# Kernel optimization log

Hardware: AMD Instinct MI355X
Metric: run time of the kernel (lower is better)

## Reference

```python
import jax, jax.numpy as jnp
import numpy as np

B, W, KD, NC, D, NN, NH, AD, HOPS = 512, 4, 64, 32, 256, 16, 8, 32, 4
DH = D // NH
DFF = 4 * D
P = B * W + B
ROLE_WRITER, ROLE_QUERY = 0, 1


def setup_inputs() -> dict:
    key = jax.random.key(0)
    ks = iter(jax.random.split(key, 40))
    f = lambda shape, s=0.02: jax.random.normal(next(ks), shape, dtype=jnp.float32) * s
    inp = {
        'query_keys': jax.random.normal(next(ks), (B, KD), dtype=jnp.float32),
        'writer_keys': jax.random.normal(next(ks), (B, W, KD), dtype=jnp.float32),
        'key_proj_w': f((KD, D)), 'key_proj_b': jnp.zeros((D,), jnp.float32),
        'class_embed': f((NC, D)), 'role_embed': f((3, D)), 'start_node_embed': f((NN, D)),
        'input_ln_g': jnp.ones((D,), jnp.float32), 'input_ln_b': jnp.zeros((D,), jnp.float32),
        'ln1_g': jnp.ones((NN, D), jnp.float32), 'ln1_b': jnp.zeros((NN, D), jnp.float32),
        'wqkv': f((NN, D, 3 * D)), 'bqkv': jnp.zeros((NN, 3 * D), jnp.float32),
        'wo': f((NN, D, D)), 'bo': jnp.zeros((NN, D), jnp.float32),
        'ln2_g': jnp.ones((NN, D), jnp.float32), 'ln2_b': jnp.zeros((NN, D), jnp.float32),
        'w_fc1': f((NN, D, DFF)), 'b_fc1': jnp.zeros((NN, DFF), jnp.float32),
        'w_fc2': f((NN, DFF, D)), 'b_fc2': jnp.zeros((NN, D), jnp.float32),
        'delta_w': jnp.zeros((D, D), jnp.float32), 'delta_b': jnp.zeros((D,), jnp.float32),
        'dir_w': f((D, D)), 'dir_b': jnp.zeros((D,), jnp.float32),
        'mag_w': f((D, 1)), 'mag_b': jnp.full((1,), 2.5, jnp.float32),
        'out_w': f((D, NC)), 'out_b': jnp.zeros((NC,), jnp.float32),
        'address_table': jax.random.normal(next(ks), (NN, AD), dtype=jnp.float32),
        'query_start_nodes': jax.random.randint(next(ks), (B,), 0, NN),
        'writer_labels': jax.random.randint(next(ks), (B, W), 0, NC),
        'writer_start_nodes': jax.random.randint(next(ks), (B, W), 0, NN),
    }
    return inp


def _ln(x):
    m = jnp.mean(x, -1, keepdims=True)
    v = jnp.var(x, -1, keepdims=True)
    return (x - m) * jax.lax.rsqrt(v + 1e-5)


def _forward(query_keys, writer_keys, key_proj_w, key_proj_b, class_embed, role_embed,
             start_node_embed, input_ln_g, input_ln_b, ln1_g, ln1_b, wqkv, bqkv, wo, bo,
             ln2_g, ln2_b, w_fc1, b_fc1, w_fc2, b_fc2, delta_w, delta_b, dir_w, dir_b,
             mag_w, mag_b, out_w, out_b, address_table,
             query_start_nodes, writer_labels, writer_start_nodes):
    # ---- encode writers (encode_writers) ----
    fk = writer_keys.reshape(-1, KD)          # [B*W, KD]
    fl = writer_labels.reshape(-1)            # [B*W]
    fs = writer_start_nodes.reshape(-1)       # [B*W]
    learned_w = fk @ key_proj_w + key_proj_b + class_embed[fl] + start_node_embed[fs] + role_embed[ROLE_WRITER]
    sw = jnp.zeros_like(learned_w).at[:, :KD].set(fk)
    sw = sw.at[:, KD:KD + NC].set(jax.nn.one_hot(fl, NC, dtype=learned_w.dtype))
    enc_w = _ln(learned_w) * input_ln_g + input_ln_b + sw
    # ---- encode queries (encode_queries) ----
    learned_q = query_keys @ key_proj_w + key_proj_b + start_node_embed[query_start_nodes] + role_embed[ROLE_QUERY]
    sq = jnp.zeros_like(learned_q).at[:, :KD].set(query_keys)
    enc_q = _ln(learned_q) * input_ln_g + input_ln_b + sq

    h = jnp.concatenate([enc_w, enc_q], axis=0)          # [P, D]
    node = jnp.concatenate([fs, query_start_nodes], 0)   # [P] current compute node per packet

    inv_sqrt_dh = 1.0 / np.sqrt(DH).astype(np.float32)
    for _ in range(HOPS):
        oh = jax.nn.one_hot(node, NN, dtype=h.dtype)      # [P, NN] dispatch weights

        def pnl(x, Wn, bn):
            # per-node linear: gather-compute-scatter via MoE-style dense dispatch
            xe = jnp.einsum('pn,pd->npd', oh, x)          # [NN, P, din]
            ye = jnp.einsum('npd,ndf->npf', xe, Wn)       # [NN, P, dout]
            return jnp.einsum('npf,pn->pf', ye, oh) + oh @ bn

        # ComputeNodeCell: pre-LN attention among packets at the same node
        x = _ln(h) * (oh @ ln1_g) + oh @ ln1_b
        qkv = pnl(x, wqkv, bqkv)                          # [P, 3D]
        q, k, v = jnp.split(qkv, 3, axis=-1)
        q = q.reshape(P, NH, DH); k = k.reshape(P, NH, DH); v = v.reshape(P, NH, DH)
        scores = jnp.einsum('phd,qhd->hpq', q, k) * inv_sqrt_dh   # [NH, P, P]
        same = node[:, None] == node[None, :]
        scores = jnp.where(same[None], scores, -1e9)
        attn = jax.nn.softmax(scores, axis=-1)
        ao = jnp.einsum('hpq,qhd->phd', attn, v).reshape(P, D)
        h = h + pnl(ao, wo, bo)
        # MLP block
        x2 = _ln(h) * (oh @ ln2_g) + oh @ ln2_b
        h = h + pnl(jax.nn.gelu(pnl(x2, w_fc1, b_fc1)), w_fc2, b_fc2)
        # routing heads: pick next node from address table, apply gated delta
        direction = h @ dir_w + dir_b
        node = jnp.argmax(direction[:, :AD] @ address_table.T, axis=-1)
        h = h + (h @ delta_w + delta_b) * jax.nn.sigmoid(h @ mag_w + mag_b)

    return h @ out_w + out_b                              # [P, NC] per-packet logits


def reference(query_keys, writer_keys, key_proj_w, key_proj_b, class_embed, role_embed,
              start_node_embed, input_ln_g, input_ln_b, ln1_g, ln1_b, wqkv, bqkv, wo, bo,
              ln2_g, ln2_b, w_fc1, b_fc1, w_fc2, b_fc2, delta_w, delta_b, dir_w, dir_b,
              mag_w, mag_b, out_w, out_b, address_table,
              query_start_nodes, writer_labels, writer_start_nodes):
    return _forward(query_keys, writer_keys, key_proj_w, key_proj_b, class_embed, role_embed,
                    start_node_embed, input_ln_g, input_ln_b, ln1_g, ln1_b, wqkv, bqkv, wo, bo,
                    ln2_g, ln2_b, w_fc1, b_fc1, w_fc2, b_fc2, delta_w, delta_b, dir_w, dir_b,
                    mag_w, mag_b, out_w, out_b, address_table,
                    query_start_nodes, writer_labels, writer_start_nodes)
```

## Files before the change

### kernel.cpp

```cpp
#include <hip/hip_runtime.h>
#include <math.h>

#define B_    512
#define W_    4
#define KD_   64
#define NC_   32
#define D_    256
#define NN_   16
#define NH_   8
#define AD_   32
#define HOPS_ 4
#define DH_   32
#define DFF_  1024
#define P_    2560
#define BW_   2048
#define MAXT2_ 176
#define PS_   (P_ + 16)

#define INV_SQRT_DH 0.17677669529663687f

typedef __attribute__((ext_vector_type(8))) short short8v;
typedef __attribute__((ext_vector_type(4))) float f32x4;

__device__ __forceinline__ unsigned short bf16_rne(float f) {
  unsigned u = __float_as_uint(f);
  unsigned r = (u + 0x7fffu + ((u >> 16) & 1u)) >> 16;
  return (unsigned short)r;
}
__device__ __forceinline__ void split2(float v, unsigned short& h, unsigned short& l) {
  unsigned short hb = bf16_rne(v);
  float hf = __uint_as_float(((unsigned)hb) << 16);
  h = hb;
  l = bf16_rne(v - hf);
}

__device__ __forceinline__ float block_sum256(float v, float* red) {
#pragma unroll
  for (int off = 32; off > 0; off >>= 1) v += __shfl_xor(v, off, 64);
  int wid = threadIdx.x >> 6;
  if ((threadIdx.x & 63) == 0) red[wid] = v;
  __syncthreads();
  float s = red[0] + red[1] + red[2] + red[3];
  __syncthreads();
  return s;
}

__device__ __forceinline__ float gelu_tanh(float v) {
  float u = 0.7978845608028654f * (v + 0.044715f * v * v * v);
  return 0.5f * v * (1.0f + tanhf(u));
}

__global__ __launch_bounds__(256) void padzero_kernel(unsigned short* __restrict__ xh,
                                                      unsigned short* __restrict__ xl,
                                                      unsigned short* __restrict__ ffh,
                                                      unsigned short* __restrict__ ffl) {
  int t = threadIdx.x;
  for (int i = t; i < 16 * D_; i += 256) {
    xh[(size_t)P_ * D_ + i] = 0;
    xl[(size_t)P_ * D_ + i] = 0;
  }
  for (int i = t; i < 16 * DFF_; i += 256) {
    ffh[(size_t)P_ * DFF_ + i] = 0;
    ffl[(size_t)P_ * DFF_ + i] = 0;
  }
}

__global__ __launch_bounds__(256) void encode_kernel(
    const float* __restrict__ query_keys, const float* __restrict__ writer_keys,
    const float* __restrict__ kpw, const float* __restrict__ kpb,
    const float* __restrict__ ce, const float* __restrict__ re,
    const float* __restrict__ sne, const float* __restrict__ ilg,
    const float* __restrict__ ilb, const int* __restrict__ qsn,
    const int* __restrict__ wl, const int* __restrict__ wsn,
    float* __restrict__ h, int* __restrict__ node) {
  int p = blockIdx.x, t = threadIdx.x;
  __shared__ float fk[KD_];
  __shared__ float red[4];
  const float* key;
  int lab = -1, sn, role;
  if (p < BW_) { key = writer_keys + (size_t)p * KD_; lab = wl[p]; sn = wsn[p]; role = 0; }
  else { int b = p - BW_; key = query_keys + (size_t)b * KD_; sn = qsn[b]; role = 1; }
  if (t < KD_) fk[t] = key[t];
  __syncthreads();

  float acc = kpb[t] + sne[sn * D_ + t] + re[role * D_ + t];
  if (lab >= 0) acc += ce[lab * D_ + t];
#pragma unroll 8
  for (int i = 0; i < KD_; i++) acc += fk[i] * kpw[i * D_ + t];

  float mean = block_sum256(acc, red) * (1.0f / D_);
  float d = acc - mean;
  float var = block_sum256(d * d, red) * (1.0f / D_);
  float xn = d * (1.0f / sqrtf(var + 1e-5f));

  float sw = 0.0f;
  if (t < KD_) sw = fk[t];
  else if (lab >= 0 && t < KD_ + NC_) sw = (t - KD_ == lab) ? 1.0f : 0.0f;

  h[(size_t)p * D_ + t] = xn * ilg[t] + ilb[t] + sw;
  if (t == 0) node[p] = sn;
}

__global__ __launch_bounds__(256) void sort_kernel(const int* __restrict__ node,
                                                   int* __restrict__ order,
                                                   int* __restrict__ offs,
                                                   int* __restrict__ cnts,
                                                   int* __restrict__ tnode16,
                                                   int* __restrict__ tstart16,
                                                   int* __restrict__ tend16,
                                                   int* __restrict__ ntiles16) {
  __shared__ int c[NN_], o[NN_], cur[NN_];
  int t = threadIdx.x;
  if (t < NN_) c[t] = 0;
  __syncthreads();
  for (int p = t; p < P_; p += 256) atomicAdd(&c[node[p]], 1);
  __syncthreads();
  if (t == 0) {
    int s = 0;
    for (int n = 0; n < NN_; n++) { o[n] = s; cur[n] = s; s += c[n]; }
    int i16 = 0;
    for (int n = 0; n < NN_; n++) {
      int e = o[n] + c[n];
      for (int m0 = o[n]; m0 < e; m0 += 16) {
        tnode16[i16] = n; tstart16[i16] = m0; tend16[i16] = e; i16++;
      }
    }
    ntiles16[0] = i16;
  }
  __syncthreads();
  if (t < NN_) { cnts[t] = c[t]; offs[t] = o[t]; }
  for (int p = t; p < P_; p += 256) {
    int r = atomicAdd(&cur[node[p]], 1);
    order[r] = p;
  }
}

__global__ __launch_bounds__(256) void ln_affine(const float* __restrict__ h,
                                                 const float* __restrict__ g,
                                                 const float* __restrict__ b,
                                                 const int* __restrict__ node,
                                                 const int* __restrict__ order,
                                                 unsigned short* __restrict__ xh,
                                                 unsigned short* __restrict__ xl) {
  int sp = blockIdx.x * 4 + (threadIdx.x >> 6);
  int lane = threadIdx.x & 63;
  int p = order[sp];
  int n = node[p];
  float4 v = *(const float4*)&h[(size_t)p * D_ + lane * 4];
  float s = v.x + v.y + v.z + v.w;
#pragma unroll
  for (int off = 32; off > 0; off >>= 1) s += __shfl_xor(s, off, 64);
  float mean = s * (1.0f / D_);
  float4 d = make_float4(v.x - mean, v.y - mean, v.z - mean, v.w - mean);
  float vr = d.x * d.x + d.y * d.y + d.z * d.z + d.w * d.w;
#pragma unroll
  for (int off = 32; off > 0; off >>= 1) vr += __shfl_xor(vr, off, 64);
  float inv = 1.0f / sqrtf(vr * (1.0f / D_) + 1e-5f);
  float4 gg = *(const float4*)&g[n * D_ + lane * 4];
  float4 bb = *(const float4*)&b[n * D_ + lane * 4];
  float o[4];
  o[0] = d.x * inv * gg.x + bb.x;
  o[1] = d.y * inv * gg.y + bb.y;
  o[2] = d.z * inv * gg.z + bb.z;
  o[3] = d.w * inv * gg.w + bb.w;
  ushort4 oh, ol;
  split2(o[0], oh.x, ol.x);
  split2(o[1], oh.y, ol.y);
  split2(o[2], oh.z, ol.z);
  split2(o[3], oh.w, ol.w);
  *(ushort4*)&xh[(size_t)sp * D_ + lane * 4] = oh;
  *(ushort4*)&xl[(size_t)sp * D_ + lane * 4] = ol;
}

template <int K, int C>
__global__ __launch_bounds__(256) void wprep(const float* __restrict__ W,
                                             unsigned short* __restrict__ th,
                                             unsigned short* __restrict__ tl) {
  __shared__ float ld[32][33];
  int n = blockIdx.z;
  int k0 = blockIdx.x * 32, c0 = blockIdx.y * 32;
  int tx = threadIdx.x & 31, ty = threadIdx.x >> 5;
  const float* Wn = W + (size_t)n * K * C;
#pragma unroll
  for (int i = 0; i < 32; i += 8)
    ld[i + ty][tx] = Wn[(size_t)(k0 + i + ty) * C + c0 + tx];
  __syncthreads();
#pragma unroll
  for (int i = 0; i < 32; i += 8) {
    float v = ld[tx][i + ty];
    unsigned short hh, ll;
    split2(v, hh, ll);
    size_t off = ((size_t)n * C + c0 + i + ty) * K + k0 + tx;
    th[off] = hh;
    tl[off] = ll;
  }
}

template <int DIN, int DOUT, int ACT, int RESID, int SPLITOUT, int DENSE, int HSPLIT>
__global__ __launch_bounds__(256) void gmfma(
    const unsigned short* __restrict__ xh, const unsigned short* __restrict__ xl,
    const unsigned short* __restrict__ wth, const unsigned short* __restrict__ wtl,
    const float* __restrict__ bias, float* __restrict__ outf,
    unsigned short* __restrict__ outh, unsigned short* __restrict__ outl,
    unsigned short* __restrict__ houth, unsigned short* __restrict__ houtl,
    const int* __restrict__ order, const int* __restrict__ tnode,
    const int* __restrict__ tstart, const int* __restrict__ tend,
    const int* __restrict__ ntiles) {
  constexpr int NCH = DIN / 64;
  __shared__ unsigned short ws[2][2][64][64];

  int gx = gridDim.x;
  int bid = blockIdx.x;
  int ti = (bid & 7) * (gx >> 3) + (bid >> 3);
  int n, s0, rows;
  if (DENSE) {
    n = 0;
    s0 = ti * 16;
    rows = 16;
  } else {
    if (ti >= ntiles[0]) return;
    n = tnode[ti];
    s0 = tstart[ti];
    rows = tend[ti] - s0;
    if (rows <= 0) return;
    if (rows > 16) rows = 16;
  }

  int tid = threadIdx.x;
  int wv = tid >> 6;
  int lane = tid & 63;
  int r16 = lane & 15;
  int kg = lane >> 4;
  int jb = blockIdx.y * 64;

  const unsigned short* wsrc[4];
  int sj[4], c0j[4];
#pragma unroll
  for (int jj = 0; jj < 4; jj++) {
    int j = wv * 4 + jj;
    int s = j >> 3;
    int c0 = (j & 7) * 8;
    int c = c0 + (lane >> 3);
    int e = (lane & 7) ^ (c & 7);
    wsrc[jj] = ((e & 4) ? wtl : wth) +
               ((size_t)(n * DOUT + jb + c)) * DIN + s * 32 + (e & 3) * 8;
    sj[jj] = s;
    c0j[jj] = c0;
  }
  auto stage = [&](int buf, int kbase) {
#pragma unroll
    for (int jj = 0; jj < 4; jj++) {
      __builtin_amdgcn_global_load_lds(
          (const __attribute__((address_space(1))) unsigned int*)(wsrc[jj] + kbase),
          (__attribute__((address_space(3))) unsigned int*)&ws[buf][sj[jj]][c0j[jj]][0],
          16, 0, 0);
    }
  };

  const unsigned short* pah = xh + (size_t)(s0 + r16) * DIN + kg * 8;
  const unsigned short* pal = xl + (size_t)(s0 + r16) * DIN + kg * 8;

  short8v ah[2], al[2], nh[2], nl[2];
  auto afetch = [&](int kbase, short8v (&h_)[2], short8v (&l_)[2]) {
#pragma unroll
    for (int s = 0; s < 2; s++) {
      h_[s] = *(const short8v*)(pah + kbase + s * 32);
      l_[s] = *(const short8v*)(pal + kbase + s * 32);
    }
  };

  f32x4 acc0 = {0.f, 0.f, 0.f, 0.f};
  f32x4 acc1 = acc0, acc2 = acc0;
  int lcol = wv * 16 + r16;
  int ghi_ = (kg ^ (r16 & 7)) * 8;
  int glo_ = ((4 + kg) ^ (r16 & 7)) * 8;

  stage(0, 0);
  afetch(0, ah, al);
  __syncthreads();

  for (int ch = 0; ch < NCH; ch++) {
    int cur = ch & 1;
    if (ch + 1 < NCH) {
      stage(cur ^ 1, (ch + 1) * 64);
      afetch((ch + 1) * 64, nh, nl);
    }
#pragma unroll
    for (int s = 0; s < 2; s++) {
      short8v bh = *(const short8v*)&ws[cur][s][lcol][ghi_];
      short8v bl = *(const short8v*)&ws[cur][s][lcol][glo_];
      acc0 = __builtin_amdgcn_mfma_f32_16x16x32_bf16(ah[s], bh, acc0, 0, 0, 0);
      acc1 = __builtin_amdgcn_mfma_f32_16x16x32_bf16(ah[s], bl, acc1, 0, 0, 0);
      acc2 = __builtin_amdgcn_mfma_f32_16x16x32_bf16(al[s], bh, acc2, 0, 0, 0);
    }
    __syncthreads();
    if (ch + 1 < NCH) {
#pragma unroll
      for (int s = 0; s < 2; s++) { ah[s] = nh[s]; al[s] = nl[s]; }
    }
  }

  int jcol = jb + wv * 16;
  float bv = bias[(size_t)n * DOUT + jcol + r16];
#pragma unroll
  for (int rg = 0; rg < 4; rg++) {
    int r = kg * 4 + rg;
    if (r >= rows) continue;
    float v = acc0[rg] + acc1[rg] + acc2[rg] + bv;
    if (ACT) v = gelu_tanh(v);
    if (SPLITOUT) {
      size_t off = (size_t)(s0 + r) * DOUT + jcol + r16;
      unsigned short hh, ll;
      split2(v, hh, ll);
      outh[off] = hh;
      outl[off] = ll;
    } else if (RESID) {
      int pp = DENSE ? (s0 + r) : order[s0 + r];
      size_t oidx = (size_t)pp * DOUT + jcol + r16;
      float nv = outf[oidx] + v;
      outf[oidx] = nv;
      if (HSPLIT) {
        unsigned short hh, ll;
        split2(nv, hh, ll);
        houth[oidx] = hh;
        houtl[oidx] = ll;
      }
    } else {
      outf[(size_t)(s0 + r) * DOUT + jcol + r16] = v;
    }
  }
}

#define ATS 36
__global__ __launch_bounds__(256) void attn_kernel(const float* __restrict__ qkv,
                                                   const int* __restrict__ node,
                                                   const int* __restrict__ order,
                                                   const int* __restrict__ offs,
                                                   const int* __restrict__ cnts,
                                                   unsigned short* __restrict__ aoh,
                                                   unsigned short* __restrict__ aol) {
  __shared__ float qs[32 * ATS];
  __shared__ float kts[2][32 * ATS];
  __shared__ float vs[2][32 * ATS];
  __shared__ float ps[32 * ATS];
  __shared__ int glo[32], ghi[32];

  int t = threadIdx.x;
  int r = t >> 3;
  int j4 = (t & 7) * 4;
  int r0 = blockIdx.x * 32;
  int hd = blockIdx.y;

  if (t < 32) {
    int n = node[order[r0 + t]];
    glo[t] = offs[n];
    ghi[t] = offs[n] + cnts[n];
  }
  __syncthreads();

  {
    const float* qp = &qkv[(size_t)(r0 + r) * 768 + hd * 32 + j4];
    float4 q4 = *(const float4*)qp;
    q4.x *= INV_SQRT_DH; q4.y *= INV_SQRT_DH; q4.z *= INV_SQRT_DH; q4.w *= INV_SQRT_DH;
    *(float4*)&qs[r * ATS + j4] = q4;
  }

  int lo = glo[0];
  int hi = ghi[31];
  int myglo = glo[r], myghi = ghi[r];
  int nt = (hi - lo + 31) >> 5;

  {
    int sj = lo + r;
    float4 k4 = {0.f, 0.f, 0.f, 0.f}, v4 = {0.f, 0.f, 0.f, 0.f};
    if (sj < hi) {
      const float* kp = &qkv[(size_t)sj * 768 + 256 + hd * 32 + j4];
      k4 = *(const float4*)kp;
      v4 = *(const float4*)(kp + 256);
    }
    kts[0][(j4 + 0) * ATS + r] = k4.x;
    kts[0][(j4 + 1) * ATS + r] = k4.y;
    kts[0][(j4 + 2) * ATS + r] = k4.z;
    kts[0][(j4 + 3) * ATS + r] = k4.w;
    *(float4*)&vs[0][r * ATS + j4] = v4;
  }
  __syncthreads();

  float4 o4 = {0.f, 0.f, 0.f, 0.f};
  float mrow = -1e30f, lrow = 0.f;

  for (int it = 0; it < nt; ++it) {
    int cb = it & 1;
    int kt = lo + it * 32;
    bool more = (it + 1 < nt);

    float4 kn = {0.f, 0.f, 0.f, 0.f}, vn = {0.f, 0.f, 0.f, 0.f};
    if (more) {
      int sj = kt + 32 + r;
      if (sj < hi) {
        const float* kp = &qkv[(size_t)sj * 768 + 256 + hd * 32 + j4];
        kn = *(const float4*)kp;
        vn = *(const float4*)(kp + 256);
      }
    }

    float s0 = 0.f, s1 = 0.f, s2 = 0.f, s3 = 0.f;
#pragma unroll 8
    for (int d = 0; d < 32; d++) {
      float qv = qs[r * ATS + d];
      float4 kv = *(const float4*)&kts[cb][d * ATS + j4];
      s0 += qv * kv.x; s1 += qv * kv.y; s2 += qv * kv.z; s3 += qv * kv.w;
    }
    int c0 = kt + j4;
    if (c0 + 0 < myglo || c0 + 0 >= myghi) s0 = -1e30f;
    if (c0 + 1 < myglo || c0 + 1 >= myghi) s1 = -1e30f;
    if (c0 + 2 < myglo || c0 + 2 >= myghi) s2 = -1e30f;
    if (c0 + 3 < myglo || c0 + 3 >= myghi) s3 = -1e30f;

    float mx = fmaxf(fmaxf(s0, s1), fmaxf(s2, s3));
#pragma unroll
    for (int off = 4; off > 0; off >>= 1) mx = fmaxf(mx, __shfl_xor(mx, off, 8));
    float mnew = fmaxf(mrow, mx);
    float alpha = __expf(mrow - mnew);
    float p0 = __expf(s0 - mnew), p1 = __expf(s1 - mnew);
    float p2 = __expf(s2 - mnew), p3 = __expf(s3 - mnew);
    float ls = p0 + p1 + p2 + p3;
#pragma unroll
    for (int off = 4; off > 0; off >>= 1) ls += __shfl_xor(ls, off, 8);
    lrow = lrow * alpha + ls;
    mrow = mnew;
    o4.x *= alpha; o4.y *= alpha; o4.z *= alpha; o4.w *= alpha;

    *(float4*)&ps[r * ATS + j4] = make_float4(p0, p1, p2, p3);
#pragma unroll 8
    for (int j = 0; j < 32; j++) {
      float pj = ps[r * ATS + j];
      float4 vv = *(const float4*)&vs[cb][j * ATS + j4];
      o4.x += pj * vv.x; o4.y += pj * vv.y; o4.z += pj * vv.z; o4.w += pj * vv.w;
    }

    if (more) {
      kts[cb ^ 1][(j4 + 0) * ATS + r] = kn.x;
      kts[cb ^ 1][(j4 + 1) * ATS + r] = kn.y;
      kts[cb ^ 1][(j4 + 2) * ATS + r] = kn.z;
      kts[cb ^ 1][(j4 + 3) * ATS + r] = kn.w;
      *(float4*)&vs[cb ^ 1][r * ATS + j4] = vn;
      __syncthreads();
    }
  }

  float inv = 1.f / lrow;
  o4.x *= inv; o4.y *= inv; o4.z *= inv; o4.w *= inv;
  ushort4 oh4, ol4;
  split2(o4.x, oh4.x, ol4.x);
  split2(o4.y, oh4.y, ol4.y);
  split2(o4.z, oh4.z, ol4.z);
  split2(o4.w, oh4.w, ol4.w);
  size_t off = (size_t)(r0 + r) * D_ + hd * 32 + j4;
  *(ushort4*)&aoh[off] = oh4;
  *(ushort4*)&aol[off] = ol4;
}

__global__ __launch_bounds__(256) void route_kernel(float* __restrict__ h,
                                                    const float* __restrict__ dir_w,
                                                    const float* __restrict__ dir_b,
                                                    const float* __restrict__ at,
                                                    const float* __restrict__ mag_w,
                                                    const float* __restrict__ mag_b,
                                                    const float* __restrict__ delta,
                                                    int* __restrict__ node) {
  int p = blockIdx.x, t = threadIdx.x;
  __shared__ float hs[D_];
  __shared__ float dpart[8][AD_];
  __shared__ float dirs[AD_];
  __shared__ float scs[NN_];
  __shared__ float red[4];
  float hv = h[(size_t)p * D_ + t];
  hs[t] = hv;
  __syncthreads();

  int j = t & 31, seg = t >> 5;
  float part = 0.0f;
#pragma unroll 8
  for (int i = 0; i < 32; i++) {
    int ii = seg * 32 + i;
    part += hs[ii] * dir_w[ii * D_ + j];
  }
  dpart[seg][j] = part;
  __syncthreads();
  if (t < AD_) {
    float s = dir_b[t];
#pragma unroll
    for (int g = 0; g < 8; g++) s += dpart[g][t];
    dirs[t] = s;
  }
  __syncthreads();
  if (t < NN_) {
    float s = 0.0f;
#pragma unroll
    for (int a = 0; a < AD_; a++) s += dirs[a] * at[t * AD_ + a];
    scs[t] = s;
  }
  __syncthreads();
  if (t == 0) {
    float best = scs[0];
    int arg = 0;
    for (int nn = 1; nn < NN_; nn++)
      if (scs[nn] > best) { best = scs[nn]; arg = nn; }
    node[p] = arg;
  }
  float mag = block_sum256(hv * mag_w[t], red) + mag_b[0];
  float sig = 1.0f / (1.0f + __expf(-mag));
  h[(size_t)p * D_ + t] = hv + delta[(size_t)p * D_ + t] * sig;
}

__global__ __launch_bounds__(256) void out_kernel(const float* __restrict__ h,
                                                  const float* __restrict__ ow,
                                                  const float* __restrict__ ob,
                                                  float* __restrict__ out) {
  int p = blockIdx.x, t = threadIdx.x;
  __shared__ float hs[D_];
  __shared__ float part[8][NC_];
  hs[t] = h[(size_t)p * D_ + t];
  __syncthreads();
  int j = t & 31, seg = t >> 5;
  float s = 0.0f;
#pragma unroll 8
  for (int i = 0; i < 32; i++) {
    int ii = seg * 32 + i;
    s += hs[ii] * ow[ii * NC_ + j];
  }
  part[seg][j] = s;
  __syncthreads();
  if (t < NC_) {
    float r = ob[t];
#pragma unroll
    for (int g = 0; g < 8; g++) r += part[g][t];
    out[(size_t)p * NC_ + t] = r;
  }
}

extern "C" void kernel_launch(void* const* d_in, const int* in_sizes, int n_in,
                              void* d_out, int out_size, void* d_ws, size_t ws_size,
                              hipStream_t stream) {
  (void)in_sizes; (void)n_in; (void)out_size; (void)ws_size;
  const float* query_keys       = (const float*)d_in[0];
  const float* writer_keys      = (const float*)d_in[1];
  const float* key_proj_w       = (const float*)d_in[2];
  const float* key_proj_b       = (const float*)d_in[3];
  const float* class_embed      = (const float*)d_in[4];
  const float* role_embed       = (const float*)d_in[5];
  const float* start_node_embed = (const float*)d_in[6];
  const float* input_ln_g       = (const float*)d_in[7];
  const float* input_ln_b       = (const float*)d_in[8];
  const float* ln1_g            = (const float*)d_in[9];
  const float* ln1_b            = (const float*)d_in[10];
  const float* wqkv             = (const float*)d_in[11];
  const float* bqkv             = (const float*)d_in[12];
  const float* wo               = (const float*)d_in[13];
  const float* bo               = (const float*)d_in[14];
  const float* ln2_g            = (const float*)d_in[15];
  const float* ln2_b            = (const float*)d_in[16];
  const float* w_fc1            = (const float*)d_in[17];
  const float* b_fc1            = (const float*)d_in[18];
  const float* w_fc2            = (const float*)d_in[19];
  const float* b_fc2            = (const float*)d_in[20];
  const float* delta_w          = (const float*)d_in[21];
  const float* delta_b          = (const float*)d_in[22];
  const float* dir_w            = (const float*)d_in[23];
  const float* dir_b            = (const float*)d_in[24];
  const float* mag_w            = (const float*)d_in[25];
  const float* mag_b            = (const float*)d_in[26];
  const float* out_w            = (const float*)d_in[27];
  const float* out_b            = (const float*)d_in[28];
  const float* address_table    = (const float*)d_in[29];
  const int* query_start_nodes  = (const int*)d_in[30];
  const int* writer_labels      = (const int*)d_in[31];
  const int* writer_start_nodes = (const int*)d_in[32];

  uintptr_t basep = (uintptr_t)d_ws;
  auto carve = [&](size_t bytes) {
    basep = (basep + 255) & ~(uintptr_t)255;
    void* r = (void*)basep;
    basep += bytes;
    return r;
  };
  float* h    = (float*)carve((size_t)P_ * D_ * 4);
  float* buf1 = (float*)carve((size_t)P_ * 768 * 4);
  unsigned short* xh  = (unsigned short*)carve((size_t)PS_ * D_ * 2);
  unsigned short* xl  = (unsigned short*)carve((size_t)PS_ * D_ * 2);
  unsigned short* ffh = (unsigned short*)carve((size_t)PS_ * DFF_ * 2);
  unsigned short* ffl = (unsigned short*)carve((size_t)PS_ * DFF_ * 2);
  unsigned short* hh  = (unsigned short*)carve((size_t)P_ * D_ * 2);
  unsigned short* hl  = (unsigned short*)carve((size_t)P_ * D_ * 2);
  unsigned short* wtqh = (unsigned short*)carve((size_t)NN_ * 768 * 256 * 2);
  unsigned short* wtql = (unsigned short*)carve((size_t)NN_ * 768 * 256 * 2);
  unsigned short* wt1h = (unsigned short*)carve((size_t)NN_ * 1024 * 256 * 2);
  unsigned short* wt1l = (unsigned short*)carve((size_t)NN_ * 1024 * 256 * 2);
  unsigned short* wt2h = (unsigned short*)carve((size_t)NN_ * 256 * 1024 * 2);
  unsigned short* wt2l = (unsigned short*)carve((size_t)NN_ * 256 * 1024 * 2);
  unsigned short* wtoh = (unsigned short*)carve((size_t)NN_ * 256 * 256 * 2);
  unsigned short* wtol = (unsigned short*)carve((size_t)NN_ * 256 * 256 * 2);
  unsigned short* dth  = (unsigned short*)carve((size_t)256 * 256 * 2);
  unsigned short* dtl  = (unsigned short*)carve((size_t)256 * 256 * 2);
  int* node   = (int*)carve(P_ * 4);
  int* order  = (int*)carve(P_ * 4);
  int* offs   = (int*)carve(NN_ * 4);
  int* cnts   = (int*)carve(NN_ * 4);
  int* tnode16  = (int*)carve(MAXT2_ * 4);
  int* tstart16 = (int*)carve(MAXT2_ * 4);
  int* tend16   = (int*)carve(MAXT2_ * 4);
  int* ntiles16 = (int*)carve(4);

  padzero_kernel<<<1, 256, 0, stream>>>(xh, xl, ffh, ffl);
  wprep<256, 768><<<dim3(8, 24, NN_), 256, 0, stream>>>(wqkv, wtqh, wtql);
  wprep<256, 1024><<<dim3(8, 32, NN_), 256, 0, stream>>>(w_fc1, wt1h, wt1l);
  wprep<1024, 256><<<dim3(32, 8, NN_), 256, 0, stream>>>(w_fc2, wt2h, wt2l);
  wprep<256, 256><<<dim3(8, 8, NN_), 256, 0, stream>>>(wo, wtoh, wtol);
  wprep<256, 256><<<dim3(8, 8, 1), 256, 0, stream>>>(delta_w, dth, dtl);

  encode_kernel<<<P_, 256, 0, stream>>>(query_keys, writer_keys, key_proj_w, key_proj_b,
                                        class_embed, role_embed, start_node_embed,
                                        input_ln_g, input_ln_b, query_start_nodes,
                                        writer_labels, writer_start_nodes, h, node);

  for (int hop = 0; hop < HOPS_; ++hop) {
    sort_kernel<<<1, 256, 0, stream>>>(node, order, offs, cnts,
                                       tnode16, tstart16, tend16, ntiles16);
    ln_affine<<<P_ / 4, 256, 0, stream>>>(h, ln1_g, ln1_b, node, order, xh, xl);
    gmfma<256, 768, 0, 0, 0, 0, 0><<<dim3(MAXT2_, 12), 256, 0, stream>>>(
        xh, xl, wtqh, wtql, bqkv, buf1, nullptr, nullptr, nullptr, nullptr,
        order, tnode16, tstart16, tend16, ntiles16);
    attn_kernel<<<dim3(P_ / 32, NH_), 256, 0, stream>>>(buf1, node, order, offs,
                                                        cnts, xh, xl);
    gmfma<256, 256, 0, 1, 0, 0, 0><<<dim3(MAXT2_, 4), 256, 0, stream>>>(
        xh, xl, wtoh, wtol, bo, h, nullptr, nullptr, nullptr, nullptr,
        order, tnode16, tstart16, tend16, ntiles16);
    ln_affine<<<P_ / 4, 256, 0, stream>>>(h, ln2_g, ln2_b, node, order, xh, xl);
    gmfma<256, 1024, 1, 0, 1, 0, 0><<<dim3(MAXT2_, 16), 256, 0, stream>>>(
        xh, xl, wt1h, wt1l, b_fc1, nullptr, ffh, ffl, nullptr, nullptr,
        order, tnode16, tstart16, tend16, ntiles16);
    gmfma<1024, 256, 0, 1, 0, 0, 1><<<dim3(MAXT2_, 4), 256, 0, stream>>>(
        ffh, ffl, wt2h, wt2l, b_fc2, h, nullptr, nullptr, hh, hl,
        order, tnode16, tstart16, tend16, ntiles16);
    gmfma<256, 256, 0, 0, 0, 1, 0><<<dim3(P_ / 16, 4), 256, 0, stream>>>(
        hh, hl, dth, dtl, delta_b, buf1, nullptr, nullptr, nullptr, nullptr,
        order, tnode16, tstart16, tend16, ntiles16);
    route_kernel<<<P_, 256, 0, stream>>>(h, dir_w, dir_b, address_table,
                                         mag_w, mag_b, buf1, node);
  }

  out_kernel<<<P_, 256, 0, stream>>>(h, out_w, out_b, (float*)d_out);
}
```

Measured before the change: 876.3 us.

## Double row tile to 32 per block with 8 waves sharing staged weights

Changes the grouped MFMA GEMMs from 16-row to 32-row tiles, using 512-thread blocks. Two groups of four waves each take 16 rows and share the same LDS-staged weight chunk, so each weight byte loaded serves twice as many rows. The per-node tile schedule, the padding rows and the grid sizes are updated to match. In exchange there are fewer blocks to fill the GPU, and partial tiles at node boundaries waste more rows.

After: 904.7 us. +3.2%, slower.

```diff
diff --git a/kernel.cpp b/kernel.cpp
--- a/kernel.cpp
+++ b/kernel.cpp
@@ -14,8 +14,8 @@
 #define DFF_  1024
 #define P_    2560
 #define BW_   2048
-#define MAXT2_ 176
-#define PS_   (P_ + 16)
+#define MAXT3_ 96
+#define PS_   (P_ + 32)
 
 #define INV_SQRT_DH 0.17677669529663687f
 
@@ -55,11 +55,11 @@
                                                       unsigned short* __restrict__ ffh,
                                                       unsigned short* __restrict__ ffl) {
   int t = threadIdx.x;
-  for (int i = t; i < 16 * D_; i += 256) {
+  for (int i = t; i < 32 * D_; i += 256) {
     xh[(size_t)P_ * D_ + i] = 0;
     xl[(size_t)P_ * D_ + i] = 0;
   }
-  for (int i = t; i < 16 * DFF_; i += 256) {
+  for (int i = t; i < 32 * DFF_; i += 256) {
     ffh[(size_t)P_ * DFF_ + i] = 0;
     ffl[(size_t)P_ * DFF_ + i] = 0;
   }
@@ -105,10 +105,10 @@
                                                    int* __restrict__ order,
                                                    int* __restrict__ offs,
                                                    int* __restrict__ cnts,
-                                                   int* __restrict__ tnode16,
-                                                   int* __restrict__ tstart16,
-                                                   int* __restrict__ tend16,
-                                                   int* __restrict__ ntiles16) {
+                                                   int* __restrict__ tnode32,
+                                                   int* __restrict__ tstart32,
+                                                   int* __restrict__ tend32,
+                                                   int* __restrict__ ntiles32) {
   __shared__ int c[NN_], o[NN_], cur[NN_];
   int t = threadIdx.x;
   if (t < NN_) c[t] = 0;
@@ -118,14 +118,14 @@
   if (t == 0) {
     int s = 0;
     for (int n = 0; n < NN_; n++) { o[n] = s; cur[n] = s; s += c[n]; }
-    int i16 = 0;
+    int i32 = 0;
     for (int n = 0; n < NN_; n++) {
       int e = o[n] + c[n];
-      for (int m0 = o[n]; m0 < e; m0 += 16) {
-        tnode16[i16] = n; tstart16[i16] = m0; tend16[i16] = e; i16++;
+      for (int m0 = o[n]; m0 < e; m0 += 32) {
+        tnode32[i32] = n; tstart32[i32] = m0; tend32[i32] = e; i32++;
       }
     }
-    ntiles16[0] = i16;
+    ntiles32[0] = i32;
   }
   __syncthreads();
   if (t < NN_) { cnts[t] = c[t]; offs[t] = o[t]; }
@@ -197,7 +197,7 @@
 }
 
 template <int DIN, int DOUT, int ACT, int RESID, int SPLITOUT, int DENSE, int HSPLIT>
-__global__ __launch_bounds__(256) void gmfma(
+__global__ __launch_bounds__(512) void gmfma(
     const unsigned short* __restrict__ xh, const unsigned short* __restrict__ xl,
     const unsigned short* __restrict__ wth, const unsigned short* __restrict__ wtl,
     const float* __restrict__ bias, float* __restrict__ outf,
@@ -215,29 +215,31 @@
   int n, s0, rows;
   if (DENSE) {
     n = 0;
-    s0 = ti * 16;
-    rows = 16;
+    s0 = ti * 32;
+    rows = 32;
   } else {
     if (ti >= ntiles[0]) return;
     n = tnode[ti];
     s0 = tstart[ti];
     rows = tend[ti] - s0;
     if (rows <= 0) return;
-    if (rows > 16) rows = 16;
+    if (rows > 32) rows = 32;
   }
 
   int tid = threadIdx.x;
   int wv = tid >> 6;
+  int rh = wv >> 2;
+  int wq = wv & 3;
   int lane = tid & 63;
   int r16 = lane & 15;
   int kg = lane >> 4;
   int jb = blockIdx.y * 64;
 
-  const unsigned short* wsrc[4];
-  int sj[4], c0j[4];
-#pragma unroll
-  for (int jj = 0; jj < 4; jj++) {
-    int j = wv * 4 + jj;
+  const unsigned short* wsrc[2];
+  int sj[2], c0j[2];
+#pragma unroll
+  for (int jj = 0; jj < 2; jj++) {
+    int j = wv * 2 + jj;
     int s = j >> 3;
     int c0 = (j & 7) * 8;
     int c = c0 + (lane >> 3);
@@ -249,7 +251,7 @@
   }
   auto stage = [&](int buf, int kbase) {
 #pragma unroll
-    for (int jj = 0; jj < 4; jj++) {
+    for (int jj = 0; jj < 2; jj++) {
       __builtin_amdgcn_global_load_lds(
           (const __attribute__((address_space(1))) unsigned int*)(wsrc[jj] + kbase),
           (__attribute__((address_space(3))) unsigned int*)&ws[buf][sj[jj]][c0j[jj]][0],
@@ -257,8 +259,8 @@
     }
   };
 
-  const unsigned short* pah = xh + (size_t)(s0 + r16) * DIN + kg * 8;
-  const unsigned short* pal = xl + (size_t)(s0 + r16) * DIN + kg * 8;
+  const unsigned short* pah = xh + (size_t)(s0 + rh * 16 + r16) * DIN + kg * 8;
+  const unsigned short* pal = xl + (size_t)(s0 + rh * 16 + r16) * DIN + kg * 8;
 
   short8v ah[2], al[2], nh[2], nl[2];
   auto afetch = [&](int kbase, short8v (&h_)[2], short8v (&l_)[2]) {
@@ -271,7 +273,7 @@
 
   f32x4 acc0 = {0.f, 0.f, 0.f, 0.f};
   f32x4 acc1 = acc0, acc2 = acc0;
-  int lcol = wv * 16 + r16;
+  int lcol = wq * 16 + r16;
   int ghi_ = (kg ^ (r16 & 7)) * 8;
   int glo_ = ((4 + kg) ^ (r16 & 7)) * 8;
 
@@ -300,11 +302,11 @@
     }
   }
 
-  int jcol = jb + wv * 16;
+  int jcol = jb + wq * 16;
   float bv = bias[(size_t)n * DOUT + jcol + r16];
 #pragma unroll
   for (int rg = 0; rg < 4; rg++) {
-    int r = kg * 4 + rg;
+    int r = rh * 16 + kg * 4 + rg;
     if (r >= rows) continue;
     float v = acc0[rg] + acc1[rg] + acc2[rg] + bv;
     if (ACT) v = gelu_tanh(v);
@@ -607,10 +609,10 @@
   int* order  = (int*)carve(P_ * 4);
   int* offs   = (int*)carve(NN_ * 4);
   int* cnts   = (int*)carve(NN_ * 4);
-  int* tnode16  = (int*)carve(MAXT2_ * 4);
-  int* tstart16 = (int*)carve(MAXT2_ * 4);
-  int* tend16   = (int*)carve(MAXT2_ * 4);
-  int* ntiles16 = (int*)carve(4);
+  int* tnode32  = (int*)carve(MAXT3_ * 4);
+  int* tstart32 = (int*)carve(MAXT3_ * 4);
+  int* tend32   = (int*)carve(MAXT3_ * 4);
+  int* ntiles32 = (int*)carve(4);
 
   padzero_kernel<<<1, 256, 0, stream>>>(xh, xl, ffh, ffl);
   wprep<256, 768><<<dim3(8, 24, NN_), 256, 0, stream>>>(wqkv, wtqh, wtql);
@@ -626,26 +628,26 @@
 
   for (int hop = 0; hop < HOPS_; ++hop) {
     sort_kernel<<<1, 256, 0, stream>>>(node, order, offs, cnts,
-                                       tnode16, tstart16, tend16, ntiles16);
+                                       tnode32, tstart32, tend32, ntiles32);
     ln_affine<<<P_ / 4, 256, 0, stream>>>(h, ln1_g, ln1_b, node, order, xh, xl);
-    gmfma<256, 768, 0, 0, 0, 0, 0><<<dim3(MAXT2_, 12), 256, 0, stream>>>(
+    gmfma<256, 768, 0, 0, 0, 0, 0><<<dim3(MAXT3_, 12), 512, 0, stream>>>(
         xh, xl, wtqh, wtql, bqkv, buf1, nullptr, nullptr, nullptr, nullptr,
-        order, tnode16, tstart16, tend16, ntiles16);
+        order, tnode32, tstart32, tend32, ntiles32);
     attn_kernel<<<dim3(P_ / 32, NH_), 256, 0, stream>>>(buf1, node, order, offs,
                                                         cnts, xh, xl);
-    gmfma<256, 256, 0, 1, 0, 0, 0><<<dim3(MAXT2_, 4), 256, 0, stream>>>(
+    gmfma<256, 256, 0, 1, 0, 0, 0><<<dim3(MAXT3_, 4), 512, 0, stream>>>(
         xh, xl, wtoh, wtol, bo, h, nullptr, nullptr, nullptr, nullptr,
-        order, tnode16, tstart16, tend16, ntiles16);
+        order, tnode32, tstart32, tend32, ntiles32);
     ln_affine<<<P_ / 4, 256, 0, stream>>>(h, ln2_g, ln2_b, node, order, xh, xl);
-    gmfma<256, 1024, 1, 0, 1, 0, 0><<<dim3(MAXT2_, 16), 256, 0, stream>>>(
+    gmfma<256, 1024, 1, 0, 1, 0, 0><<<dim3(MAXT3_, 16), 512, 0, stream>>>(
         xh, xl, wt1h, wt1l, b_fc1, nullptr, ffh, ffl, nullptr, nullptr,
-        order, tnode16, tstart16, tend16, ntiles16);
-    gmfma<1024, 256, 0, 1, 0, 0, 1><<<dim3(MAXT2_, 4), 256, 0, stream>>>(
+        order, tnode32, tstart32, tend32, ntiles32);
+    gmfma<1024, 256, 0, 1, 0, 0, 1><<<dim3(MAXT3_, 4), 512, 0, stream>>>(
         ffh, ffl, wt2h, wt2l, b_fc2, h, nullptr, nullptr, hh, hl,
-        order, tnode16, tstart16, tend16, ntiles16);
-    gmfma<256, 256, 0, 0, 0, 1, 0><<<dim3(P_ / 16, 4), 256, 0, stream>>>(
+        order, tnode32, tstart32, tend32, ntiles32);
+    gmfma<256, 256, 0, 0, 0, 1, 0><<<dim3(P_ / 32, 4), 512, 0, stream>>>(
         hh, hl, dth, dtl, delta_b, buf1, nullptr, nullptr, nullptr, nullptr,
-        order, tnode16, tstart16, tend16, ntiles16);
+        order, tnode32, tstart32, tend32, ntiles32);
     route_kernel<<<P_, 256, 0, stream>>>(h, dir_w, dir_b, address_table,
                                          mag_w, mag_b, buf1, node);
   }
```
